# Kernel tuning notes

Measured on AMD Instinct MI355X. Metric: run time of the kernel, lower is better.

Reference implementation:

```python
import jax, jax.numpy as jnp
import numpy as np

H = 16        # num_heads (= num_v_heads)
D = 128       # head_k_dim
DV = 128      # head_v_dim (expand_v = 1)
R = 4         # micro_rank
CONV = 4      # short conv kernel size
EPS = 1e-5    # o_norm eps
FILL = -10000.0  # micro_fill_g_raw


def setup_inputs() -> dict:
    key = jax.random.key(0)
    ks = jax.random.split(key, 16)
    B, T, HID = 2, 1024, 2048
    KD, VD = H * D, H * DV
    w = lambda k, shape, s=0.02: (jax.random.normal(k, shape, jnp.float32) * s)
    micro_logits = jnp.full((H, R), -8.0, jnp.float32).at[:, -1].set(0.0)
    return {
        'hidden_states': jax.random.normal(ks[0], (B, T, HID), jnp.float32),
        'q_proj_w': w(ks[1], (KD, HID)),
        'k_proj_w': w(ks[2], (KD * R, HID)),
        'v_proj_w': w(ks[3], (VD * R, HID)),
        'q_conv_w': w(ks[4], (KD, CONV), 0.3),
        'k_conv_w': w(ks[5], (KD * R, CONV), 0.3),
        'v_conv_w': w(ks[6], (VD * R, CONV), 0.3),
        'f1_w': w(ks[7], (DV, HID)),
        'f2_w': w(ks[8], (KD, DV)),
        'b_proj_w': w(ks[9], (H * R, HID)),
        'micro_logits': micro_logits,
        'A_log': jnp.log(jax.random.uniform(ks[10], (H,), jnp.float32, 1.0, 16.0)),
        'dt_bias': jnp.zeros((KD,), jnp.float32),
        'g1_w': w(ks[11], (DV, HID)),
        'g2_w': w(ks[12], (VD, DV)),
        'g2_b': jnp.zeros((VD,), jnp.float32),
        'o_norm_w': jnp.ones((DV,), jnp.float32),
        'o_proj_w': w(ks[13], (HID, VD)),
    }


def _short_conv(x, w):
    # causal depthwise conv1d + silu; x: [B,T,C], w: [C,K]
    K = w.shape[1]
    T = x.shape[1]
    xp = jnp.pad(x, ((0, 0), (K - 1, 0), (0, 0)))
    out = sum(xp[:, i:i + T, :] * w[:, i] for i in range(K))
    return jax.nn.silu(out)


def _l2norm(x):
    return x * jax.lax.rsqrt(jnp.sum(x * x, -1, keepdims=True) + 1e-6)


def _forward(hidden_states, q_proj_w, k_proj_w, v_proj_w, q_conv_w, k_conv_w,
             v_conv_w, f1_w, f2_w, b_proj_w, micro_logits, A_log, dt_bias,
             g1_w, g2_w, g2_b, o_norm_w, o_proj_w):
    B, T, _ = hidden_states.shape
    x = hidden_states
    q = _short_conv(x @ q_proj_w.T, q_conv_w).reshape(B, T, H, D)
    k = _short_conv(x @ k_proj_w.T, k_conv_w).reshape(B, T, H, R, D)
    v = _short_conv(x @ v_proj_w.T, v_conv_w).reshape(B, T, H, R, DV)
    # fused_kda_gate: g = -exp(A_log) * softplus(g_raw + dt_bias), per head/channel
    g_raw = (x @ f1_w.T) @ f2_w.T                      # [B,T,H*D]
    A = jnp.exp(A_log)[:, None]                        # [H,1]
    g = -A * jax.nn.softplus(g_raw.reshape(B, T, H, D) + dt_bias.reshape(H, D))
    beta = jax.nn.sigmoid(x @ b_proj_w.T).reshape(B, T, H, R)
    # KDA kernels apply qk l2-norm in kernel, plus 1/sqrt(Dk) query scale
    q = _l2norm(q) * (D ** -0.5)
    k = _l2norm(k)
    decay0 = jnp.exp(g)                                # token-level per-channel decay (micro-step 0)
    decay_fill = jnp.exp(-A * jax.nn.softplus(FILL + dt_bias.reshape(H, D)))  # ~1, [H,D]

    def step(S, inp):
        # S: [B,H,D,DV]; r serial rank-1 delta updates per token
        q_t, k_t, v_t, b_t, d_t = inp
        outs = []
        for j in range(R):
            d = d_t if j == 0 else jnp.broadcast_to(decay_fill, d_t.shape)
            S = S * d[..., None]
            kj, vj, bj = k_t[:, :, j], v_t[:, :, j], b_t[:, :, j]
            u = jnp.einsum('bhd,bhdv->bhv', kj, S)
            S = S + (bj[..., None] * kj)[..., None] * (vj - u)[..., None, :]
            outs.append(jnp.einsum('bhd,bhdv->bhv', q_t, S))
        return S, jnp.stack(outs, axis=-2)              # [B,H,R,DV]

    S0 = jnp.zeros((B, H, D, DV), q.dtype)
    xs = (jnp.swapaxes(q, 0, 1), jnp.swapaxes(k, 0, 1), jnp.swapaxes(v, 0, 1),
          jnp.swapaxes(beta, 0, 1), jnp.swapaxes(decay0, 0, 1))
    _, o_micro = jax.lax.scan(step, S0, xs)             # [T,B,H,R,DV]
    wmix = jax.nn.softmax(micro_logits, axis=-1)        # [H,R] micro-readout mix
    o = jnp.einsum('tbhrv,hr->bthv', o_micro, wmix)
    # gated RMSNorm (sigmoid gate) then output projection
    gate = ((x @ g1_w.T) @ g2_w.T + g2_b).reshape(B, T, H, DV)
    o = o * jax.lax.rsqrt(jnp.mean(o * o, -1, keepdims=True) + EPS)
    o = o * o_norm_w * jax.nn.sigmoid(gate)
    return o.reshape(B, T, H * DV) @ o_proj_w.T


def reference(hidden_states, q_proj_w, k_proj_w, v_proj_w, q_conv_w, k_conv_w,
              v_conv_w, f1_w, f2_w, b_proj_w, micro_logits, A_log, dt_bias,
              g1_w, g2_w, g2_b, o_norm_w, o_proj_w):
    return _forward(hidden_states, q_proj_w, k_proj_w, v_proj_w, q_conv_w,
                    k_conv_w, v_conv_w, f1_w, f2_w, b_proj_w, micro_logits,
                    A_log, dt_bias, g1_w, g2_w, g2_b, o_norm_w, o_proj_w)
```

## Files before the change

### kernel.cpp

```cpp
#include <hip/hip_runtime.h>
#include <hip/hip_bf16.h>
#include <math.h>


typedef unsigned short ushort_t;
typedef __attribute__((ext_vector_type(8))) short bf16x8;
typedef __attribute__((ext_vector_type(4))) float f32x4;
typedef __attribute__((ext_vector_type(8))) unsigned short u16x8;

__device__ __forceinline__ unsigned short f2bf(float f) {
  unsigned u = __float_as_uint(f);
  unsigned r = (u + 0x7FFFu + ((u >> 16) & 1u)) >> 16;
  return (unsigned short)r;
}
__device__ __forceinline__ unsigned f2bf_pk(float lo, float hi) {
  unsigned r;
  asm("v_cvt_pk_bf16_f32 %0, %1, %2" : "=v"(r) : "v"(lo), "v"(hi));
  return r;
}
__device__ __forceinline__ float bf2f(unsigned short u) {
  return __uint_as_float(((unsigned)u) << 16);
}
__device__ __forceinline__ float sigmoidf(float x) { return 1.f / (1.f + expf(-x)); }
__device__ __forceinline__ float softplusf(float x) {
  return (x > 20.f) ? x : log1pf(expf(x));
}
__device__ __forceinline__ void store1(float* p, float v) { *p = v; }
__device__ __forceinline__ void store1(unsigned short* p, float v) {
  *p = (unsigned short)f2bf_pk(v, v);
}

template <typename OutT>
__global__ __launch_bounds__(256) void gemm_mfma(const float* __restrict__ A,
                                                 const float* __restrict__ B,
                                                 OutT* __restrict__ Y,
                                                 int M, int N, int K) {
  __shared__ __attribute__((aligned(16))) unsigned short As[128 * 40];
  __shared__ __attribute__((aligned(16))) unsigned short Bs[128 * 40];
  const int tid = threadIdx.x;
  const int lane = tid & 63;
  const int wave = tid >> 6;
  const int quad = lane >> 4;
  const int l16 = lane & 15;
  const int wm = wave >> 1;
  const int wn = wave & 1;
  const int n0 = blockIdx.x * 128;
  const int m0 = blockIdx.y * 128;

  f32x4 acc[4][4];
#pragma unroll
  for (int i = 0; i < 4; ++i)
#pragma unroll
    for (int j = 0; j < 4; ++j) acc[i][j] = (f32x4){0.f, 0.f, 0.f, 0.f};

  for (int k0 = 0; k0 < K; k0 += 32) {
    __syncthreads();
#pragma unroll
    for (int u = tid; u < 512; u += 256) {
      int m = u >> 2, c = u & 3;
      const float* src = A + (size_t)(m0 + m) * K + k0 + c * 8;
      float4 a0 = *(const float4*)(src);
      float4 a1 = *(const float4*)(src + 4);
      *(uint2*)&As[m * 40 + c * 8] =
          make_uint2(f2bf_pk(a0.x, a0.y), f2bf_pk(a0.z, a0.w));
      *(uint2*)&As[m * 40 + c * 8 + 4] =
          make_uint2(f2bf_pk(a1.x, a1.y), f2bf_pk(a1.z, a1.w));
    }
#pragma unroll
    for (int u = tid; u < 512; u += 256) {
      int n = u >> 2, c = u & 3;
      float4 b0 = make_float4(0.f, 0.f, 0.f, 0.f);
      float4 b1 = b0;
      if (n0 + n < N) {
        const float* src = B + (size_t)(n0 + n) * K + k0 + c * 8;
        b0 = *(const float4*)(src);
        b1 = *(const float4*)(src + 4);
      }
      *(uint2*)&Bs[n * 40 + c * 8] =
          make_uint2(f2bf_pk(b0.x, b0.y), f2bf_pk(b0.z, b0.w));
      *(uint2*)&Bs[n * 40 + c * 8 + 4] =
          make_uint2(f2bf_pk(b1.x, b1.y), f2bf_pk(b1.z, b1.w));
    }
    __syncthreads();

    bf16x8 av[4], bv[4];
#pragma unroll
    for (int i = 0; i < 4; ++i)
      av[i] = *(const bf16x8*)&As[(wm * 64 + i * 16 + l16) * 40 + quad * 8];
#pragma unroll
    for (int j = 0; j < 4; ++j)
      bv[j] = *(const bf16x8*)&Bs[(wn * 64 + j * 16 + l16) * 40 + quad * 8];
#pragma unroll
    for (int i = 0; i < 4; ++i)
#pragma unroll
      for (int j = 0; j < 4; ++j)
        acc[i][j] = __builtin_amdgcn_mfma_f32_16x16x32_bf16(av[i], bv[j], acc[i][j], 0, 0, 0);
  }

#pragma unroll
  for (int i = 0; i < 4; ++i)
#pragma unroll
    for (int j = 0; j < 4; ++j) {
      int rr = m0 + wm * 64 + i * 16 + quad * 4;
      int cc = n0 + wn * 64 + j * 16 + l16;
      if (cc < N) {
#pragma unroll
        for (int r = 0; r < 4; ++r)
          store1(Y + (size_t)(rr + r) * N + cc, acc[i][j][r]);
      }
    }
}

__global__ __launch_bounds__(256) void conv_silu_v8(const unsigned short* __restrict__ X,
                                                    const float* __restrict__ Wc,
                                                    unsigned short* __restrict__ Y,
                                                    int C, int total8) {
  int i8 = blockIdx.x * 256 + threadIdx.x;
  if (i8 >= total8) return;
  int idx = i8 * 8;
  int c = idx % C;
  int m = idx / C;
  int t = m & 1023;
  u16x8 x0 = *(const u16x8*)(X + idx);
  u16x8 x1 = (u16x8)(unsigned short)0;
  u16x8 x2 = x1, x3 = x1;
  if (t >= 1) x1 = *(const u16x8*)(X + idx - C);
  if (t >= 2) x2 = *(const u16x8*)(X + idx - 2 * C);
  if (t >= 3) x3 = *(const u16x8*)(X + idx - 3 * C);
  float r[8];
#pragma unroll
  for (int e = 0; e < 8; ++e) {
    float4 w4 = *(const float4*)(Wc + (size_t)(c + e) * 4);
    float acc = w4.w * bf2f(x0[e]);
    acc = fmaf(w4.z, bf2f(x1[e]), acc);
    acc = fmaf(w4.y, bf2f(x2[e]), acc);
    acc = fmaf(w4.x, bf2f(x3[e]), acc);
    r[e] = acc * sigmoidf(acc);
  }
  *(uint4*)(Y + idx) = make_uint4(f2bf_pk(r[0], r[1]), f2bf_pk(r[2], r[3]),
                                  f2bf_pk(r[4], r[5]), f2bf_pk(r[6], r[7]));
}

__global__ __launch_bounds__(256) void l2norm_bf16(unsigned short* __restrict__ X,
                                                   int rows, float post) {
  int row = blockIdx.x * 4 + (threadIdx.x >> 6);
  int lane = threadIdx.x & 63;
  if (row >= rows) return;
  unsigned short* p = X + (size_t)row * 128;
  float a = bf2f(p[lane]), b = bf2f(p[lane + 64]);
  float ss = fmaf(a, a, b * b);
#pragma unroll
  for (int m = 32; m; m >>= 1) ss += __shfl_xor(ss, m);
  float sc = rsqrtf(ss + 1e-6f) * post;
  p[lane] = f2bf(a * sc);
  p[lane + 64] = f2bf(b * sc);
}

__global__ __launch_bounds__(256) void decay_ip(float* __restrict__ G,
                                                const float* __restrict__ alog,
                                                const float* __restrict__ dtb,
                                                int total) {
  int idx = blockIdx.x * 256 + threadIdx.x;
  if (idx >= total) return;
  int n = idx & 2047;
  float A = expf(alog[n >> 7]);
  float x = G[idx] + dtb[n];
  G[idx] = expf(-A * softplusf(x));
}

__global__ __launch_bounds__(256) void sigmoid_ip(float* __restrict__ G, int total) {
  int idx = blockIdx.x * 256 + threadIdx.x;
  if (idx < total) G[idx] = sigmoidf(G[idx]);
}

template <int CTRL>
__device__ __forceinline__ float dppadd(float x) {
  int y = __builtin_amdgcn_update_dpp(0, __float_as_int(x), CTRL, 0xF, 0xF, true);
  return x + __int_as_float(y);
}
__device__ __forceinline__ float red64_l63(float x) {
  x = dppadd<0xB1>(x);
  x = dppadd<0x4E>(x);
  x = dppadd<0x141>(x);
  x = dppadd<0x140>(x);
  x = dppadd<0x142>(x);
  x = dppadd<0x143>(x);
  return x;
}
__device__ __forceinline__ float red64(float x) {
  return __int_as_float(__builtin_amdgcn_readlane(__float_as_int(red64_l63(x)), 63));
}

struct Pref {
  ushort2 k[4];
  ushort2 q;
  float2 d;
  float4 beta;
  unsigned short v[4];
};

__global__ __launch_bounds__(256) void scan_kernel6(
    const unsigned short* __restrict__ Qn, const unsigned short* __restrict__ Kn,
    const unsigned short* __restrict__ Vb, const float* __restrict__ Dec,
    const float* __restrict__ BetaS, const float* __restrict__ ml,
    const float* __restrict__ alog, const float* __restrict__ dtb,
    float* __restrict__ O) {
  const int orig = blockIdx.x;
  const int xcd = orig & 7;
  const int rr = orig >> 3;
  const int bh = xcd * 4 + (rr & 3);
  const int cq = rr >> 2;
  const int h = bh & 15;
  const int b = bh >> 4;
  const int wave = threadIdx.x >> 6;
  const int lane = threadIdx.x & 63;
  const int col = cq * 4 + wave;
  const int d0 = lane * 2;

  const float A = expf(alog[h]);
  const float df0 = expf(-A * softplusf(-10000.f + dtb[h * 128 + d0]));
  const float df1 = expf(-A * softplusf(-10000.f + dtb[h * 128 + d0 + 1]));

  float wj[4];
  {
    float l0 = ml[h * 4 + 0], l1 = ml[h * 4 + 1];
    float l2 = ml[h * 4 + 2], l3 = ml[h * 4 + 3];
    float mx = fmaxf(fmaxf(l0, l1), fmaxf(l2, l3));
    float e0 = expf(l0 - mx), e1 = expf(l1 - mx);
    float e2 = expf(l2 - mx), e3 = expf(l3 - mx);
    float inv = 1.f / (e0 + e1 + e2 + e3);
    wj[0] = e0 * inv; wj[1] = e1 * inv; wj[2] = e2 * inv; wj[3] = e3 * inv;
  }

  float S0 = 0.f, S1 = 0.f;

  auto LD = [&](int t, Pref& P) {
    const size_t base = ((size_t)(b * 1024 + t) * 16 + h);
    const unsigned short* kp = Kn + base * 512 + d0;
    const unsigned short* vp = Vb + base * 512 + col;
#pragma unroll
    for (int j = 0; j < 4; ++j) {
      P.k[j] = *(const ushort2*)(kp + j * 128);
      P.v[j] = vp[j * 128];
    }
    P.q = *(const ushort2*)(Qn + base * 128 + d0);
    P.d = *(const float2*)(Dec + base * 128 + d0);
    P.beta = *(const float4*)(BetaS + base * 4);
  };

  auto STEP = [&](const Pref& P, int t) {
    const float qf0 = bf2f(P.q.x), qf1 = bf2f(P.q.y);
    float o_acc = 0.f;
    const float bc[4] = {P.beta.x, P.beta.y, P.beta.z, P.beta.w};
#pragma unroll
    for (int j = 0; j < 4; ++j) {
      const float kf0 = bf2f(P.k[j].x), kf1 = bf2f(P.k[j].y);
      const float dd0 = (j == 0) ? P.d.x : df0;
      const float dd1 = (j == 0) ? P.d.y : df1;
      S0 *= dd0;
      S1 *= dd1;
      float u = red64(fmaf(kf0, S0, kf1 * S1));
      float cc = bc[j] * (bf2f(P.v[j]) - u);
      S0 = fmaf(cc, kf0, S0);
      S1 = fmaf(cc, kf1, S1);
      o_acc = fmaf(wj[j], fmaf(qf0, S0, qf1 * S1), o_acc);
    }
    o_acc = red64_l63(o_acc);
    if (lane == 63) {
      const size_t base = ((size_t)(b * 1024 + t) * 16 + h);
      O[base * 128 + col] = o_acc;
    }
  };

  Pref P0, P1;
  LD(0, P0);
  for (int t = 0; t < 1024; t += 2) {
    LD(t + 1, P1);
    STEP(P0, t);
    if (t + 2 < 1024) LD(t + 2, P0);
    STEP(P1, t + 1);
  }
}

__global__ __launch_bounds__(256) void norm_gate(float* __restrict__ O,
                                                 const unsigned short* __restrict__ G,
                                                 const float* __restrict__ g2b,
                                                 const float* __restrict__ onw,
                                                 int rows) {
  int row = blockIdx.x * 4 + (threadIdx.x >> 6);
  int lane = threadIdx.x & 63;
  if (row >= rows) return;
  float* p = O + (size_t)row * 128;
  int m = row >> 4, h = row & 15;
  const unsigned short* gp = G + (size_t)m * 2048 + h * 128;
  const float* gb = g2b + h * 128;
  float a = p[lane], bv = p[lane + 64];
  float ss = fmaf(a, a, bv * bv);
#pragma unroll
  for (int k = 32; k; k >>= 1) ss += __shfl_xor(ss, k);
  float sc = rsqrtf(ss * (1.f / 128.f) + 1e-5f);
  float ga = sigmoidf(bf2f(gp[lane]) + gb[lane]);
  float gbv = sigmoidf(bf2f(gp[lane + 64]) + gb[lane + 64]);
  p[lane] = a * sc * onw[lane] * ga;
  p[lane + 64] = bv * sc * onw[lane + 64] * gbv;
}

extern "C" void kernel_launch(void* const* d_in, const int* in_sizes, int n_in,
                              void* d_out, int out_size, void* d_ws, size_t ws_size,
                              hipStream_t stream) {
  const float* x    = (const float*)d_in[0];
  const float* qw   = (const float*)d_in[1];
  const float* kw   = (const float*)d_in[2];
  const float* vw   = (const float*)d_in[3];
  const float* qcw  = (const float*)d_in[4];
  const float* kcw  = (const float*)d_in[5];
  const float* vcw  = (const float*)d_in[6];
  const float* f1w  = (const float*)d_in[7];
  const float* f2w  = (const float*)d_in[8];
  const float* bw   = (const float*)d_in[9];
  const float* ml   = (const float*)d_in[10];
  const float* alog = (const float*)d_in[11];
  const float* dtb  = (const float*)d_in[12];
  const float* g1w  = (const float*)d_in[13];
  const float* g2w  = (const float*)d_in[14];
  const float* g2b  = (const float*)d_in[15];
  const float* onw  = (const float*)d_in[16];
  const float* ow   = (const float*)d_in[17];
  float* out = (float*)d_out;

  char* w8 = (char*)d_ws;
  unsigned short* P    = (unsigned short*)(w8);
  float*          dec  = (float*)(w8);
  unsigned short* gate = (unsigned short*)(w8 + 16777216);
  float*          beta = (float*)(w8 + 25165824);
  float*          g1t  = (float*)(w8 + 25690112);
  unsigned short* Kc   = (unsigned short*)(w8 + 33554432);
  unsigned short* Vc   = (unsigned short*)(w8 + 67108864);
  unsigned short* Qc   = (unsigned short*)(w8 + 100663296);
  float*          o    = (float*)(w8 + 109051904);
  (void)ws_size;

  const int M = 2048;
  dim3 blk(256);

  gemm_mfma<unsigned short><<<dim3(64, 16), blk, 0, stream>>>(x, kw, P, M, 8192, 2048);
  conv_silu_v8<<<8192, blk, 0, stream>>>(P, kcw, Kc, 8192, 2097152);
  gemm_mfma<unsigned short><<<dim3(64, 16), blk, 0, stream>>>(x, vw, P, M, 8192, 2048);
  conv_silu_v8<<<8192, blk, 0, stream>>>(P, vcw, Vc, 8192, 2097152);
  gemm_mfma<unsigned short><<<dim3(16, 16), blk, 0, stream>>>(x, qw, P, M, 2048, 2048);
  conv_silu_v8<<<2048, blk, 0, stream>>>(P, qcw, Qc, 2048, 524288);

  gemm_mfma<float><<<dim3(1, 16), blk, 0, stream>>>(x, f1w, g1t, M, 128, 2048);
  gemm_mfma<float><<<dim3(16, 16), blk, 0, stream>>>(g1t, f2w, dec, M, 2048, 128);
  decay_ip<<<16384, blk, 0, stream>>>(dec, alog, dtb, 4194304);

  gemm_mfma<float><<<dim3(1, 16), blk, 0, stream>>>(x, bw, beta, M, 64, 2048);
  sigmoid_ip<<<512, blk, 0, stream>>>(beta, 131072);

  gemm_mfma<float><<<dim3(1, 16), blk, 0, stream>>>(x, g1w, g1t, M, 128, 2048);
  gemm_mfma<unsigned short><<<dim3(16, 16), blk, 0, stream>>>(g1t, g2w, gate, M, 2048, 128);

  l2norm_bf16<<<8192, blk, 0, stream>>>(Qc, 32768, 0.08838834764831845f);
  l2norm_bf16<<<32768, blk, 0, stream>>>(Kc, 131072, 1.0f);

  scan_kernel6<<<1024, dim3(256), 0, stream>>>(Qc, Kc, Vc, dec, beta, ml, alog, dtb, o);

  norm_gate<<<8192, blk, 0, stream>>>(o, gate, g2b, onw, 32768);

  gemm_mfma<float><<<dim3(16, 16), blk, 0, stream>>>(o, ow, out, M, 2048, 2048);
}
```

Measured before the change: 2.055 ms.

## Pre-convert GEMM operands to bf16 and use direct global-to-LDS loads

Adds a standalone fp32-to-bf16 conversion kernel and a new bf16-input GEMM that loads tiles with global_load_lds (falling back to a plain copy), using an XOR-swizzled LDS layout and a 64-wide K step. The large K/V/Q projections and the output projection now convert the activation and weight tensors to bf16 first, which halves the bytes the GEMM reads and removes per-tile conversion work inside its main loop. The cost is extra conversion passes over the weights on every call and more LDS per block. Workspace regions are reused for the converted buffers, so correctness depends on those regions not overlapping live data.

```diff
diff --git a/kernel.cpp b/kernel.cpp
--- a/kernel.cpp
+++ b/kernel.cpp
@@ -28,6 +28,101 @@
 __device__ __forceinline__ void store1(float* p, float v) { *p = v; }
 __device__ __forceinline__ void store1(unsigned short* p, float v) {
   *p = (unsigned short)f2bf_pk(v, v);
+}
+
+#if __has_builtin(__builtin_amdgcn_global_load_lds)
+__device__ __forceinline__ void gload16(const void* g, void* lds, int lane) {
+  (void)lane;
+  __builtin_amdgcn_global_load_lds(
+      (const __attribute__((address_space(1))) unsigned int*)g,
+      (__attribute__((address_space(3))) unsigned int*)lds, 16, 0, 0);
+}
+#else
+__device__ __forceinline__ void gload16(const void* g, void* lds, int lane) {
+  uint4 v = *(const uint4*)g;
+  *(uint4*)((char*)lds + lane * 16) = v;
+}
+#endif
+
+__global__ __launch_bounds__(256) void cvt_bf16_v8(const float* __restrict__ X,
+                                                   unsigned short* __restrict__ Y,
+                                                   int total8) {
+  int i = blockIdx.x * 256 + threadIdx.x;
+  if (i >= total8) return;
+  const float4* s = (const float4*)(X + (size_t)i * 8);
+  float4 a = s[0], b = s[1];
+  *(uint4*)(Y + (size_t)i * 8) = make_uint4(f2bf_pk(a.x, a.y), f2bf_pk(a.z, a.w),
+                                            f2bf_pk(b.x, b.y), f2bf_pk(b.z, b.w));
+}
+
+template <typename OutT>
+__global__ __launch_bounds__(256) void gemm_bf16(const unsigned short* __restrict__ A,
+                                                 const unsigned short* __restrict__ B,
+                                                 OutT* __restrict__ Y,
+                                                 int M, int N, int K) {
+  __shared__ __attribute__((aligned(16))) unsigned short As[128 * 64];
+  __shared__ __attribute__((aligned(16))) unsigned short Bs[128 * 64];
+  const int tid = threadIdx.x;
+  const int lane = tid & 63;
+  const int wave = tid >> 6;
+  const int quad = lane >> 4;
+  const int l16 = lane & 15;
+  const int wm = wave >> 1, wn = wave & 1;
+  const int n0 = blockIdx.x * 128;
+  const int m0 = blockIdx.y * 128;
+
+  const int srow = lane >> 3;
+  const int glog = (lane & 7) ^ (srow & 7);
+  const unsigned short* Ab = A + (size_t)(m0 + wave * 32 + srow) * K + glog * 8;
+  const unsigned short* Bb = B + (size_t)(n0 + wave * 32 + srow) * K + glog * 8;
+  unsigned short* AsW = As + wave * 2048;
+  unsigned short* BsW = Bs + wave * 2048;
+
+  f32x4 acc[4][4];
+#pragma unroll
+  for (int i = 0; i < 4; ++i)
+#pragma unroll
+    for (int j = 0; j < 4; ++j) acc[i][j] = (f32x4){0.f, 0.f, 0.f, 0.f};
+
+  for (int k0 = 0; k0 < K; k0 += 64) {
+    __syncthreads();
+#pragma unroll
+    for (int r = 0; r < 4; ++r) {
+      gload16(Ab + (size_t)(r * 8) * K + k0, AsW + r * 512, lane);
+      gload16(Bb + (size_t)(r * 8) * K + k0, BsW + r * 512, lane);
+    }
+    __syncthreads();
+#pragma unroll
+    for (int kk = 0; kk < 2; ++kk) {
+      bf16x8 av[4], bv[4];
+#pragma unroll
+      for (int i = 0; i < 4; ++i) {
+        int row = wm * 64 + i * 16 + l16;
+        av[i] = *(const bf16x8*)&As[row * 64 + (((kk * 4 + quad) ^ (row & 7)) * 8)];
+      }
+#pragma unroll
+      for (int j = 0; j < 4; ++j) {
+        int row = wn * 64 + j * 16 + l16;
+        bv[j] = *(const bf16x8*)&Bs[row * 64 + (((kk * 4 + quad) ^ (row & 7)) * 8)];
+      }
+#pragma unroll
+      for (int i = 0; i < 4; ++i)
+#pragma unroll
+        for (int j = 0; j < 4; ++j)
+          acc[i][j] = __builtin_amdgcn_mfma_f32_16x16x32_bf16(av[i], bv[j], acc[i][j], 0, 0, 0);
+    }
+  }
+
+#pragma unroll
+  for (int i = 0; i < 4; ++i)
+#pragma unroll
+    for (int j = 0; j < 4; ++j) {
+      int rr = m0 + wm * 64 + i * 16 + quad * 4;
+      int cc = n0 + wn * 64 + j * 16 + l16;
+#pragma unroll
+      for (int r = 0; r < 4; ++r)
+        store1(Y + (size_t)(rr + r) * N + cc, acc[i][j][r]);
+    }
 }
 
 template <typename OutT>
@@ -336,18 +431,28 @@
   float*          g1t  = (float*)(w8 + 25690112);
   unsigned short* Kc   = (unsigned short*)(w8 + 33554432);
   unsigned short* Vc   = (unsigned short*)(w8 + 67108864);
+  unsigned short* wbig = (unsigned short*)(w8 + 67108864);
   unsigned short* Qc   = (unsigned short*)(w8 + 100663296);
+  unsigned short* xbf  = (unsigned short*)(w8 + 109051904);
+  unsigned short* qwbf = (unsigned short*)(w8 + 117440512);
   float*          o    = (float*)(w8 + 109051904);
+  unsigned short* owbf = (unsigned short*)(w8);
+  unsigned short* obf  = (unsigned short*)(w8 + 8388608);
   (void)ws_size;
 
   const int M = 2048;
   dim3 blk(256);
 
-  gemm_mfma<unsigned short><<<dim3(64, 16), blk, 0, stream>>>(x, kw, P, M, 8192, 2048);
+  cvt_bf16_v8<<<2048, blk, 0, stream>>>(x, xbf, 524288);
+
+  cvt_bf16_v8<<<8192, blk, 0, stream>>>(kw, wbig, 2097152);
+  gemm_bf16<unsigned short><<<dim3(64, 16), blk, 0, stream>>>(xbf, wbig, P, M, 8192, 2048);
   conv_silu_v8<<<8192, blk, 0, stream>>>(P, kcw, Kc, 8192, 2097152);
-  gemm_mfma<unsigned short><<<dim3(64, 16), blk, 0, stream>>>(x, vw, P, M, 8192, 2048);
+  cvt_bf16_v8<<<8192, blk, 0, stream>>>(vw, wbig, 2097152);
+  gemm_bf16<unsigned short><<<dim3(64, 16), blk, 0, stream>>>(xbf, wbig, P, M, 8192, 2048);
   conv_silu_v8<<<8192, blk, 0, stream>>>(P, vcw, Vc, 8192, 2097152);
-  gemm_mfma<unsigned short><<<dim3(16, 16), blk, 0, stream>>>(x, qw, P, M, 2048, 2048);
+  cvt_bf16_v8<<<2048, blk, 0, stream>>>(qw, qwbf, 524288);
+  gemm_bf16<unsigned short><<<dim3(16, 16), blk, 0, stream>>>(xbf, qwbf, P, M, 2048, 2048);
   conv_silu_v8<<<2048, blk, 0, stream>>>(P, qcw, Qc, 2048, 524288);
 
   gemm_mfma<float><<<dim3(1, 16), blk, 0, stream>>>(x, f1w, g1t, M, 128, 2048);
@@ -367,5 +472,7 @@
 
   norm_gate<<<8192, blk, 0, stream>>>(o, gate, g2b, onw, 32768);
 
-  gemm_mfma<float><<<dim3(16, 16), blk, 0, stream>>>(o, ow, out, M, 2048, 2048);
-}
+  cvt_bf16_v8<<<2048, blk, 0, stream>>>(o, obf, 524288);
+  cvt_bf16_v8<<<2048, blk, 0, stream>>>(ow, owbf, 524288);
+  gemm_bf16<float><<<dim3(16, 16), blk, 0, stream>>>(obf, owbf, out, M, 2048, 2048);
+}
```

After: 1.760 ms. 1.17x faster.
